# Optimization experiments

Hardware: AMD Instinct MI355X
Metric: run time of the kernel (lower is better)

## Reference

```python
import jax, jax.numpy as jnp
import numpy as np

B, SQ, SK, D, H = 2, 2048, 2048, 1024, 16
DK = D // H


def setup_inputs() -> dict:
    key = jax.random.key(0)
    ks = jax.random.split(key, 9)
    query = jax.random.normal(ks[0], (B, SQ, D), dtype=jnp.float32)
    k_in = jax.random.normal(ks[1], (B, SK, D), dtype=jnp.float32)
    v_in = jax.random.normal(ks[2], (B, SK, D), dtype=jnp.float32)
    # padding mask: 1 for valid tokens, 0 for padding; lengths in [SK//2, SK]
    lengths = jax.random.randint(ks[3], (B,), SK // 2, SK + 1)
    mask = (jnp.arange(SK)[None, :] < lengths[:, None]).astype(jnp.int32)
    scale = 1.0 / np.sqrt(D)
    Wq = jax.random.normal(ks[4], (D, D), dtype=jnp.float32) * scale
    Wk = jax.random.normal(ks[5], (D, D), dtype=jnp.float32) * scale
    Wv = jax.random.normal(ks[6], (D, D), dtype=jnp.float32) * scale
    Wo = jax.random.normal(ks[7], (D, D), dtype=jnp.float32) * scale
    return {"query": query, "key": k_in, "value": v_in, "mask": mask,
            "Wq": Wq, "Wk": Wk, "Wv": Wv, "Wo": Wo}


def reference(query, key, value, mask, Wq, Wk, Wv, Wo):
    # linear projections (torch Linear: x @ W.T)
    q = (query @ Wq.T).reshape(B, SQ, H, DK).transpose(0, 2, 1, 3)  # [B,H,SQ,DK]
    k = (key @ Wk.T).reshape(B, SK, H, DK).transpose(0, 2, 1, 3)    # [B,H,SK,DK]
    v = (value @ Wv.T).reshape(B, SK, H, DK).transpose(0, 2, 1, 3)  # [B,H,SK,DK]
    scores = jnp.einsum('bhqd,bhkd->bhqk', q, k) / jnp.sqrt(jnp.float32(DK))
    # padding mask: (B, SK) -> (B, 1, 1, SK)
    scores = jnp.where(mask[:, None, None, :] == 0, -jnp.inf, scores)
    # future (causal) mask
    future = jnp.triu(jnp.ones((SQ, SK), dtype=bool), k=1)
    scores = jnp.where(future[None, None], -jnp.inf, scores)
    attn = jax.nn.softmax(scores, axis=-1)
    attn = jnp.nan_to_num(attn, nan=0.0)
    ctx = jnp.einsum('bhqk,bhkd->bhqd', attn, v)
    ctx = ctx.transpose(0, 2, 1, 3).reshape(B, SQ, D)
    return ctx @ Wo.T
```

## Files before the change

kernel.cpp:

```cpp
#include <hip/hip_runtime.h>
#include <hip/hip_bf16.h>
#include <stdint.h>

#define BB 2
#define SS 2048
#define DD 1024
#define HH 16
#define DKK 64
#define MM (BB*SS)
#define LOG2E 1.4426950408889634f
#define QSCALE (0.125f * LOG2E)

typedef __attribute__((ext_vector_type(8))) short short8;
typedef __attribute__((ext_vector_type(8))) _Float16 half8;
typedef __attribute__((ext_vector_type(4))) float f32x4;

__device__ __forceinline__ short bfr(float f) {
    return (short)((__float_as_uint(f) + 0x8000u) >> 16);
}
__device__ __forceinline__ short f2h(float f) {
    _Float16 h = (_Float16)f;
    return __builtin_bit_cast(short, h);
}
__device__ __forceinline__ short8 cvt8(float4 a, float4 b) {
    short8 s;
    s[0] = bfr(a.x); s[1] = bfr(a.y); s[2] = bfr(a.z); s[3] = bfr(a.w);
    s[4] = bfr(b.x); s[5] = bfr(b.y); s[6] = bfr(b.z); s[7] = bfr(b.w);
    return s;
}

__device__ __forceinline__ void dma16(const void* g, void* l) {
    __builtin_amdgcn_global_load_lds(
        (const __attribute__((address_space(1))) uint32_t*)g,
        (__attribute__((address_space(3))) uint32_t*)(uintptr_t)l, 16, 0, 0);
}


__global__ __launch_bounds__(256) void cvt_all(const float* __restrict__ q,
                                               const float* __restrict__ k,
                                               const float* __restrict__ v,
                                               const float* __restrict__ wq,
                                               const float* __restrict__ wk,
                                               const float* __restrict__ wv,
                                               const float* __restrict__ wo,
                                               const int* __restrict__ mask,
                                               short* __restrict__ dst,
                                               float* __restrict__ Fb) {
    const size_t nth = (size_t)gridDim.x * blockDim.x;
    const size_t tid = (size_t)blockIdx.x * blockDim.x + threadIdx.x;
    if (tid < BB * SS) Fb[tid] = mask[tid] ? 0.f : -30000.f;
    for (size_t i8 = tid; i8 < (1u << 21); i8 += nth) {
        const size_t e = i8 * 8;
        const float* s;
        size_t rel;
        if (e < 4194304)        { s = q; rel = e; }
        else if (e < 8388608)   { s = k; rel = e - 4194304; }
        else if (e < 12582912)  { s = v; rel = e - 8388608; }
        else {
            const size_t we = e - 12582912;
            s = (we < 1048576) ? wq : (we < 2097152) ? wk : (we < 3145728) ? wv : wo;
            rel = we & 1048575;
        }
        const float4* p = (const float4*)(s + rel);
        *(short8*)(dst + e) = cvt8(p[0], p[1]);
    }
}

__global__ __launch_bounds__(256) void qkv_lds(const short* __restrict__ Abf,
                                               const short* __restrict__ Wbf,
                                               short* __restrict__ Qb,
                                               short* __restrict__ Kb,
                                               short* __restrict__ Vtb) {
    __shared__ __align__(16) short SH[12288];
    short* As = SH;
    short* Ws = SH + 4096;
    const int z = blockIdx.z;
    const short* A = Abf + (size_t)z * 4194304;
    const short* W = Wbf + (size_t)z * 1048576;
    const int t = threadIdx.x, wave = t >> 6, lane = t & 63;
    const int la = lane & 15, quad = lane >> 4;
    const int wm = wave & 1, wn = wave >> 1;
    const int m0 = blockIdx.x * 64, n0 = blockIdx.y * 128;

    f32x4 acc[2][4];
    #pragma unroll
    for (int i = 0; i < 2; ++i)
        #pragma unroll
        for (int j = 0; j < 4; ++j) acc[i][j] = {0.f, 0.f, 0.f, 0.f};

    for (int k0 = 0; k0 < DD; k0 += 64) {
        #pragma unroll
        for (int j = 0; j < 2; ++j) {
            const int idx = j * 256 + t;
            const int row = idx >> 3, gc = (idx & 7) ^ (row & 7);
            dma16(A + (size_t)(m0 + row) * DD + k0 + gc * 8, As + idx * 8);
        }
        #pragma unroll
        for (int j = 0; j < 4; ++j) {
            const int idx = j * 256 + t;
            const int row = idx >> 3, gc = (idx & 7) ^ (row & 7);
            dma16(W + (size_t)(n0 + row) * DD + k0 + gc * 8, Ws + idx * 8);
        }
        __syncthreads();
        #pragma unroll
        for (int kh = 0; kh < 2; ++kh) {
            short8 af[2], bf[4];
            #pragma unroll
            for (int mt = 0; mt < 2; ++mt) {
                const int row = wm * 32 + mt * 16 + la;
                af[mt] = *(const short8*)&As[row * 64 + (((kh << 2) | quad) ^ (row & 7)) * 8];
            }
            #pragma unroll
            for (int nt = 0; nt < 4; ++nt) {
                const int row = wn * 64 + nt * 16 + la;
                bf[nt] = *(const short8*)&Ws[row * 64 + (((kh << 2) | quad) ^ (row & 7)) * 8];
            }
            #pragma unroll
            for (int mt = 0; mt < 2; ++mt)
                #pragma unroll
                for (int nt = 0; nt < 4; ++nt)
                    acc[mt][nt] = __builtin_amdgcn_mfma_f32_16x16x32_bf16(af[mt], bf[nt], acc[mt][nt], 0, 0, 0);
        }
        __syncthreads();
    }

    #pragma unroll
    for (int mt = 0; mt < 2; ++mt)
        #pragma unroll
        for (int nt = 0; nt < 4; ++nt)
            #pragma unroll
            for (int r = 0; r < 4; ++r) {
                const float v = acc[mt][nt][r];
                const int mr = wm * 32 + mt * 16 + quad * 4 + r;
                const int nc = wn * 64 + nt * 16 + la;
                if (z == 2) SH[nc * 68 + mr] = f2h(v);
                else        SH[mr * 132 + nc] = bfr(z == 0 ? v * QSCALE : v);
            }
    __syncthreads();

    const int b = m0 >> 11;
    #pragma unroll
    for (int p = 0; p < 4; ++p) {
        const int idx = p * 256 + t;
        if (z == 2) {
            const int rr = idx >> 3, c8 = (idx & 7) * 8;
            short8 val = *(const short8*)&SH[rr * 68 + c8];
            const int n = n0 + rr, h2 = n >> 6, dk = n & 63;
            const int s = (m0 & (SS - 1)) + c8;
            *(short8*)(Vtb + ((size_t)(b * HH + h2) * DKK + dk) * SS + s) = val;
        } else {
            const int rr = idx >> 4, c8 = (idx & 15) * 8;
            short8 val = *(const short8*)&SH[rr * 132 + c8];
            const int s = (m0 + rr) & (SS - 1);
            const int n = n0 + c8, h2 = n >> 6, dk = n & 63;
            short* Y = (z == 0) ? Qb : Kb;
            *(short8*)(Y + ((size_t)(b * HH + h2) * SS + s) * DKK + dk) = val;
        }
    }
}

__global__ __launch_bounds__(256) void attn6(const short* __restrict__ Q,
                                             const short* __restrict__ K,
                                             const short* __restrict__ Vt,
                                             const float* __restrict__ Fb,
                                             short* __restrict__ ctx) {
    const int b = blockIdx.z, h = blockIdx.y, x = blockIdx.x;
    const int qtH = 31 - x, qtL = x;
    const int t = threadIdx.x, wave = t >> 6, lane = t & 63;
    const int la = lane & 15, quad = lane >> 4;

    __shared__ __align__(16) short Ks[64 * 72];
    __shared__ __align__(16) short Vs[64 * 72];
    __shared__ __align__(16) short PsH[64 * 72];
    __shared__ __align__(16) short PsL[64 * 72];

    const size_t kbase = ((size_t)(b * HH + h) * SS) * DKK;
    const size_t vbase = ((size_t)(b * HH + h) * DKK) * SS;

    const short8 aqH0 = *(const short8*)(Q + kbase + (size_t)(qtH * 64 + wave * 16 + la) * DKK + quad * 8);
    const short8 aqH1 = *(const short8*)(Q + kbase + (size_t)(qtH * 64 + wave * 16 + la) * DKK + 32 + quad * 8);
    const short8 aqL0 = *(const short8*)(Q + kbase + (size_t)(qtL * 64 + wave * 16 + la) * DKK + quad * 8);
    const short8 aqL1 = *(const short8*)(Q + kbase + (size_t)(qtL * 64 + wave * 16 + la) * DKK + 32 + quad * 8);

    const int srow = t >> 2, scol = (t & 3) * 16;
    short8 kr[2], vr[2];
    auto loadG = [&](int kt) {
        const short* kp = K + kbase + (size_t)(kt * 64 + srow) * DKK + scol;
        kr[0] = ((const short8*)kp)[0]; kr[1] = ((const short8*)kp)[1];
        const short* vp = Vt + vbase + (size_t)srow * SS + kt * 64 + scol;
        vr[0] = ((const short8*)vp)[0]; vr[1] = ((const short8*)vp)[1];
    };
    auto storeL = [&]() {
        *(short8*)&Ks[srow * 72 + scol]     = kr[0];
        *(short8*)&Ks[srow * 72 + scol + 8] = kr[1];
        *(short8*)&Vs[srow * 72 + scol]     = vr[0];
        *(short8*)&Vs[srow * 72 + scol + 8] = vr[1];
    };

    float rsH[4] = {0.f, 0.f, 0.f, 0.f}, rsL[4] = {0.f, 0.f, 0.f, 0.f};
    f32x4 oH[4], oL[4];
    #pragma unroll
    for (int dc = 0; dc < 4; ++dc) {
        oH[dc] = {0.f, 0.f, 0.f, 0.f};
        oL[dc] = {0.f, 0.f, 0.f, 0.f};
    }

    loadG(0); storeL(); __syncthreads();

    for (int kt = 0; kt <= qtH; ++kt) {
        if (kt < qtH) loadG(kt + 1);
        const bool doL = (kt <= qtL);

        f32x4 sH[4], sL[4];
        #pragma unroll
        for (int ct = 0; ct < 4; ++ct) {
            short8 kb0 = *(const short8*)&Ks[(ct * 16 + la) * 72 + quad * 8];
            short8 kb1 = *(const short8*)&Ks[(ct * 16 + la) * 72 + 32 + quad * 8];
            sH[ct] = {0.f, 0.f, 0.f, 0.f};
            sH[ct] = __builtin_amdgcn_mfma_f32_16x16x32_bf16(aqH0, kb0, sH[ct], 0, 0, 0);
            sH[ct] = __builtin_amdgcn_mfma_f32_16x16x32_bf16(aqH1, kb1, sH[ct], 0, 0, 0);
            if (doL) {
                sL[ct] = {0.f, 0.f, 0.f, 0.f};
                sL[ct] = __builtin_amdgcn_mfma_f32_16x16x32_bf16(aqL0, kb0, sL[ct], 0, 0, 0);
                sL[ct] = __builtin_amdgcn_mfma_f32_16x16x32_bf16(aqL1, kb1, sL[ct], 0, 0, 0);
            }
        }

        {
            const bool diag = (kt == qtH);
            const bool padded = (kt >= 16);
            #pragma unroll
            for (int ct = 0; ct < 4; ++ct) {
                const int col = kt * 64 + ct * 16 + la;
                const float bias = padded ? Fb[b * SS + col] : 0.f;
                const int row0 = qtH * 64 + wave * 16 + quad * 4;
                #pragma unroll
                for (int r = 0; r < 4; ++r) {
                    float xv = sH[ct][r] + bias;
                    if (diag && col > row0 + r) xv = -30000.f;
                    const float p = exp2f(xv);
                    rsH[r] += p;
                    PsH[(wave * 16 + quad * 4 + r) * 72 + ct * 16 + la] = f2h(p);
                }
            }
        }
        if (doL) {
            const bool diag = (kt == qtL);
            #pragma unroll
            for (int ct = 0; ct < 4; ++ct) {
                const int col = kt * 64 + ct * 16 + la;
                const int row0 = qtL * 64 + wave * 16 + quad * 4;
                #pragma unroll
                for (int r = 0; r < 4; ++r) {
                    float xv = sL[ct][r];
                    if (diag && col > row0 + r) xv = -30000.f;
                    const float p = exp2f(xv);
                    rsL[r] += p;
                    PsL[(wave * 16 + quad * 4 + r) * 72 + ct * 16 + la] = f2h(p);
                }
            }
        }

        #pragma unroll
        for (int c2 = 0; c2 < 2; ++c2) {
            half8 paH = *(const half8*)&PsH[(wave * 16 + la) * 72 + c2 * 32 + quad * 8];
            half8 paL;
            if (doL) paL = *(const half8*)&PsL[(wave * 16 + la) * 72 + c2 * 32 + quad * 8];
            #pragma unroll
            for (int dc = 0; dc < 4; ++dc) {
                half8 vb = *(const half8*)&Vs[(dc * 16 + la) * 72 + c2 * 32 + quad * 8];
                oH[dc] = __builtin_amdgcn_mfma_f32_16x16x32_f16(paH, vb, oH[dc], 0, 0, 0);
                if (doL)
                    oL[dc] = __builtin_amdgcn_mfma_f32_16x16x32_f16(paL, vb, oL[dc], 0, 0, 0);
            }
        }

        if (kt < qtH) {
            __syncthreads();
            storeL();
            __syncthreads();
        }
    }

    #pragma unroll
    for (int r = 0; r < 4; ++r) {
        float v = rsH[r];
        v += __shfl_xor(v, 1, 64);
        v += __shfl_xor(v, 2, 64);
        v += __shfl_xor(v, 4, 64);
        v += __shfl_xor(v, 8, 64);
        const float inv = 1.0f / v;
        const int q = qtH * 64 + wave * 16 + quad * 4 + r;
        #pragma unroll
        for (int dc = 0; dc < 4; ++dc)
            ctx[((size_t)(b * SS + q) * DD) + h * DKK + dc * 16 + la] = bfr(oH[dc][r] * inv);
    }
    #pragma unroll
    for (int r = 0; r < 4; ++r) {
        float v = rsL[r];
        v += __shfl_xor(v, 1, 64);
        v += __shfl_xor(v, 2, 64);
        v += __shfl_xor(v, 4, 64);
        v += __shfl_xor(v, 8, 64);
        const float inv = 1.0f / v;
        const int q = qtL * 64 + wave * 16 + quad * 4 + r;
        #pragma unroll
        for (int dc = 0; dc < 4; ++dc)
            ctx[((size_t)(b * SS + q) * DD) + h * DKK + dc * 16 + la] = bfr(oL[dc][r] * inv);
    }
}

__global__ __launch_bounds__(256) void o_lds(const short* __restrict__ Ctx,
                                             const short* __restrict__ Wob,
                                             float* __restrict__ out) {
    __shared__ __align__(16) short As[64 * 64];
    __shared__ __align__(16) short Ws[64 * 64];
    const int t = threadIdx.x, wave = t >> 6, lane = t & 63;
    const int la = lane & 15, quad = lane >> 4;
    const int wm = wave & 1, wn = wave >> 1;
    const int m0 = blockIdx.x * 64, n0 = blockIdx.y * 64;

    f32x4 acc[2][2];
    #pragma unroll
    for (int i = 0; i < 2; ++i)
        #pragma unroll
        for (int j = 0; j < 2; ++j) acc[i][j] = {0.f, 0.f, 0.f, 0.f};

    for (int k0 = 0; k0 < DD; k0 += 64) {
        #pragma unroll
        for (int j = 0; j < 2; ++j) {
            const int idx = j * 256 + t;
            const int row = idx >> 3, gc = (idx & 7) ^ (row & 7);
            dma16(Ctx + (size_t)(m0 + row) * DD + k0 + gc * 8, (short*)As + idx * 8);
            dma16(Wob + (size_t)(n0 + row) * DD + k0 + gc * 8, (short*)Ws + idx * 8);
        }
        __syncthreads();
        #pragma unroll
        for (int kh = 0; kh < 2; ++kh) {
            short8 af[2], bf[2];
            #pragma unroll
            for (int mt = 0; mt < 2; ++mt) {
                const int row = wm * 32 + mt * 16 + la;
                af[mt] = *(const short8*)&As[row * 64 + (((kh << 2) | quad) ^ (row & 7)) * 8];
            }
            #pragma unroll
            for (int nt = 0; nt < 2; ++nt) {
                const int row = wn * 32 + nt * 16 + la;
                bf[nt] = *(const short8*)&Ws[row * 64 + (((kh << 2) | quad) ^ (row & 7)) * 8];
            }
            #pragma unroll
            for (int mt = 0; mt < 2; ++mt)
                #pragma unroll
                for (int nt = 0; nt < 2; ++nt)
                    acc[mt][nt] = __builtin_amdgcn_mfma_f32_16x16x32_bf16(af[mt], bf[nt], acc[mt][nt], 0, 0, 0);
        }
        __syncthreads();
    }

    #pragma unroll
    for (int mt = 0; mt < 2; ++mt)
        #pragma unroll
        for (int nt = 0; nt < 2; ++nt)
            #pragma unroll
            for (int r = 0; r < 4; ++r) {
                const int m = m0 + wm * 32 + mt * 16 + quad * 4 + r;
                const int n = n0 + wn * 32 + nt * 16 + la;
                out[(size_t)m * DD + n] = acc[mt][nt][r];
            }
}

__global__ __launch_bounds__(256) void qkv_gemm(const float* __restrict__ Aq,
                                                const float* __restrict__ Ak,
                                                const float* __restrict__ Av,
                                                const float* __restrict__ Wq,
                                                const float* __restrict__ Wk,
                                                const float* __restrict__ Wv,
                                                short* __restrict__ Qb,
                                                short* __restrict__ Kb,
                                                short* __restrict__ Vtb) {
    __shared__ __align__(16) short As[2][128][40];
    __shared__ __align__(16) short Ws[2][128][40];
    const int z = blockIdx.z;
    const float* A = (z == 0) ? Aq : (z == 1) ? Ak : Av;
    const float* W = (z == 0) ? Wq : (z == 1) ? Wk : Wv;
    short* Y = (z == 0) ? Qb : (z == 1) ? Kb : Vtb;
    const int t = threadIdx.x, wave = t >> 6, lane = t & 63;
    const int la = lane & 15, quad = lane >> 4;
    const int wm = wave & 1, wn = wave >> 1;
    const int m0 = blockIdx.x * 128, n0 = blockIdx.y * 128;
    const int srow = t >> 1, scol = (t & 1) * 16;
    f32x4 acc[4][4];
    #pragma unroll
    for (int i = 0; i < 4; ++i)
        #pragma unroll
        for (int j = 0; j < 4; ++j) acc[i][j] = {0.f, 0.f, 0.f, 0.f};
    float4 ar[4], wr[4];
    auto loadG = [&](int i) {
        const int k0 = i * 32;
        const float4* pa = (const float4*)(A + (size_t)(m0 + srow) * DD + k0 + scol);
        ar[0] = pa[0]; ar[1] = pa[1]; ar[2] = pa[2]; ar[3] = pa[3];
        const float4* pw = (const float4*)(W + (size_t)(n0 + srow) * DD + k0 + scol);
        wr[0] = pw[0]; wr[1] = pw[1]; wr[2] = pw[2]; wr[3] = pw[3];
    };
    auto storeL = [&](int buf) {
        *(short8*)&As[buf][srow][scol]     = cvt8(ar[0], ar[1]);
        *(short8*)&As[buf][srow][scol + 8] = cvt8(ar[2], ar[3]);
        *(short8*)&Ws[buf][srow][scol]     = cvt8(wr[0], wr[1]);
        *(short8*)&Ws[buf][srow][scol + 8] = cvt8(wr[2], wr[3]);
    };
    loadG(0); storeL(0); __syncthreads();
    const int NIT = DD / 32;
    for (int i = 0; i < NIT; ++i) {
        if (i + 1 < NIT) loadG(i + 1);
        const int buf = i & 1;
        short8 af[4], bfv[4];
        #pragma unroll
        for (int mt = 0; mt < 4; ++mt)
            af[mt] = *(const short8*)&As[buf][wm * 64 + mt * 16 + la][quad * 8];
        #pragma unroll
        for (int nt = 0; nt < 4; ++nt)
            bfv[nt] = *(const short8*)&Ws[buf][wn * 64 + nt * 16 + la][quad * 8];
        #pragma unroll
        for (int mt = 0; mt < 4; ++mt)
            #pragma unroll
            for (int nt = 0; nt < 4; ++nt)
                acc[mt][nt] = __builtin_amdgcn_mfma_f32_16x16x32_bf16(af[mt], bfv[nt], acc[mt][nt], 0, 0, 0);
        if (i + 1 < NIT) { storeL((i + 1) & 1); __syncthreads(); }
    }
    #pragma unroll
    for (int mt = 0; mt < 4; ++mt)
        #pragma unroll
        for (int nt = 0; nt < 4; ++nt)
            #pragma unroll
            for (int r = 0; r < 4; ++r) {
                const int m = m0 + wm * 64 + mt * 16 + quad * 4 + r;
                const int n = n0 + wn * 64 + nt * 16 + la;
                const int b = m >> 11, s = m & (SS - 1);
                const int h = n >> 6, dk = n & 63;
                float v = acc[mt][nt][r];
                if (z == 0)      Y[(((size_t)(b * HH + h) * SS + s) * DKK) + dk] = bfr(v * QSCALE);
                else if (z == 1) Y[(((size_t)(b * HH + h) * SS + s) * DKK) + dk] = bfr(v);
                else             Y[(((size_t)(b * HH + h) * DKK + dk) * SS) + s] = bfr(v);
            }
}

__global__ __launch_bounds__(256) void attn_fused(const short* __restrict__ Q,
                                                  const short* __restrict__ K,
                                                  const short* __restrict__ Vt,
                                                  const int* __restrict__ mask,
                                                  short* __restrict__ ctx) {
    const int b = blockIdx.z, h = blockIdx.y, x = blockIdx.x;
    const int t = threadIdx.x, wave = t >> 6, lane = t & 63;
    const int la = lane & 15, quad = lane >> 4;
    __shared__ __align__(16) short Ks[2][64][72];
    __shared__ __align__(16) short Vs[2][64][72];
    __shared__ __align__(16) short Ps[64][72];
    const size_t kbase = ((size_t)(b * HH + h) * SS) * DKK;
    const size_t vbase = ((size_t)(b * HH + h) * DKK) * SS;
    const int srow = t >> 2, scol = (t & 3) * 16;
    short8 kr[2], vr[2];
    auto loadG = [&](int kt) {
        const short* kp = K + kbase + (size_t)(kt * 64 + srow) * DKK + scol;
        kr[0] = ((const short8*)kp)[0]; kr[1] = ((const short8*)kp)[1];
        const short* vp = Vt + vbase + (size_t)srow * SS + kt * 64 + scol;
        vr[0] = ((const short8*)vp)[0]; vr[1] = ((const short8*)vp)[1];
    };
    auto storeL = [&](int buf) {
        *(short8*)&Ks[buf][srow][scol]     = kr[0];
        *(short8*)&Ks[buf][srow][scol + 8] = kr[1];
        *(short8*)&Vs[buf][srow][scol]     = vr[0];
        *(short8*)&Vs[buf][srow][scol + 8] = vr[1];
    };
    #pragma unroll 1
    for (int phase = 0; phase < 2; ++phase) {
        const int qt = phase ? x : (31 - x);
        const size_t qbase = kbase + (size_t)(qt * 64) * DKK;
        const short8 aq0 = *(const short8*)(Q + qbase + (size_t)(wave * 16 + la) * DKK + quad * 8);
        const short8 aq1 = *(const short8*)(Q + qbase + (size_t)(wave * 16 + la) * DKK + 32 + quad * 8);
        float rs[4] = {0.f, 0.f, 0.f, 0.f};
        f32x4 o[4];
        #pragma unroll
        for (int dc = 0; dc < 4; ++dc) o[dc] = {0.f, 0.f, 0.f, 0.f};
        const int nkt = qt + 1;
        loadG(0); storeL(0); __syncthreads();
        for (int kt = 0; kt < nkt; ++kt) {
            if (kt + 1 < nkt) loadG(kt + 1);
            const int buf = kt & 1;
            const bool diag = (kt == qt);
            const bool padded = (kt >= 16);
            f32x4 s[4];
            #pragma unroll
            for (int ct = 0; ct < 4; ++ct) {
                s[ct] = {0.f, 0.f, 0.f, 0.f};
                short8 kb0 = *(const short8*)&Ks[buf][ct * 16 + la][quad * 8];
                short8 kb1 = *(const short8*)&Ks[buf][ct * 16 + la][32 + quad * 8];
                s[ct] = __builtin_amdgcn_mfma_f32_16x16x32_bf16(aq0, kb0, s[ct], 0, 0, 0);
                s[ct] = __builtin_amdgcn_mfma_f32_16x16x32_bf16(aq1, kb1, s[ct], 0, 0, 0);
            }
            const int rowq = qt * 64 + wave * 16 + quad * 4;
            #pragma unroll
            for (int ct = 0; ct < 4; ++ct) {
                const int col = kt * 64 + ct * 16 + la;
                const int mv = padded ? mask[b * SS + col] : 1;
                #pragma unroll
                for (int r = 0; r < 4; ++r) {
                    const bool dead = (diag && col > rowq + r) || (padded && mv == 0);
                    const float p = dead ? 0.f : exp2f(s[ct][r]);
                    rs[r] += p;
                    Ps[wave * 16 + quad * 4 + r][ct * 16 + la] = bfr(p);
                }
            }
            #pragma unroll
            for (int c2 = 0; c2 < 2; ++c2) {
                short8 pa = *(const short8*)&Ps[wave * 16 + la][c2 * 32 + quad * 8];
                #pragma unroll
                for (int dc = 0; dc < 4; ++dc) {
                    short8 vb = *(const short8*)&Vs[buf][dc * 16 + la][c2 * 32 + quad * 8];
                    o[dc] = __builtin_amdgcn_mfma_f32_16x16x32_bf16(pa, vb, o[dc], 0, 0, 0);
                }
            }
            if (kt + 1 < nkt) { storeL((kt + 1) & 1); __syncthreads(); }
        }
        #pragma unroll
        for (int r = 0; r < 4; ++r) {
            float v = rs[r];
            v += __shfl_xor(v, 1, 64);
            v += __shfl_xor(v, 2, 64);
            v += __shfl_xor(v, 4, 64);
            v += __shfl_xor(v, 8, 64);
            const float inv = 1.0f / v;
            const int q = qt * 64 + wave * 16 + quad * 4 + r;
            #pragma unroll
            for (int dc = 0; dc < 4; ++dc)
                ctx[((size_t)(b * SS + q) * DD) + h * DKK + dc * 16 + la] = bfr(o[dc][r] * inv);
        }
        __syncthreads();
    }
}

__global__ __launch_bounds__(256) void o_gemm(const short* __restrict__ Ctx,
                                              const float* __restrict__ Wo,
                                              float* __restrict__ out) {
    __shared__ __align__(16) short As[2][128][40];
    __shared__ __align__(16) short Ws[2][64][40];
    const int t = threadIdx.x, wave = t >> 6, lane = t & 63;
    const int la = lane & 15, quad = lane >> 4;
    const int wm = wave & 1, wn = wave >> 1;
    const int m0 = blockIdx.x * 128, n0 = blockIdx.y * 64;
    const int srowA = t >> 1, scolA = (t & 1) * 16;
    const int srowW = t >> 2, scolW = (t & 3) * 8;
    f32x4 acc[4][2];
    #pragma unroll
    for (int i = 0; i < 4; ++i)
        #pragma unroll
        for (int j = 0; j < 2; ++j) acc[i][j] = {0.f, 0.f, 0.f, 0.f};
    short8 ab[2];
    float4 wr[2];
    auto loadG = [&](int i) {
        const int k0 = i * 32;
        const short8* pa = (const short8*)(Ctx + (size_t)(m0 + srowA) * DD + k0 + scolA);
        ab[0] = pa[0]; ab[1] = pa[1];
        const float4* pw = (const float4*)(Wo + (size_t)(n0 + srowW) * DD + k0 + scolW);
        wr[0] = pw[0]; wr[1] = pw[1];
    };
    auto storeL = [&](int buf) {
        *(short8*)&As[buf][srowA][scolA]     = ab[0];
        *(short8*)&As[buf][srowA][scolA + 8] = ab[1];
        *(short8*)&Ws[buf][srowW][scolW]     = cvt8(wr[0], wr[1]);
    };
    loadG(0); storeL(0); __syncthreads();
    const int NIT = DD / 32;
    for (int i = 0; i < NIT; ++i) {
        if (i + 1 < NIT) loadG(i + 1);
        const int buf = i & 1;
        short8 af[4], bfv[2];
        #pragma unroll
        for (int mt = 0; mt < 4; ++mt)
            af[mt] = *(const short8*)&As[buf][wm * 64 + mt * 16 + la][quad * 8];
        #pragma unroll
        for (int nt = 0; nt < 2; ++nt)
            bfv[nt] = *(const short8*)&Ws[buf][wn * 32 + nt * 16 + la][quad * 8];
        #pragma unroll
        for (int mt = 0; mt < 4; ++mt)
            #pragma unroll
            for (int nt = 0; nt < 2; ++nt)
                acc[mt][nt] = __builtin_amdgcn_mfma_f32_16x16x32_bf16(af[mt], bfv[nt], acc[mt][nt], 0, 0, 0);
        if (i + 1 < NIT) { storeL((i + 1) & 1); __syncthreads(); }
    }
    #pragma unroll
    for (int mt = 0; mt < 4; ++mt)
        #pragma unroll
        for (int nt = 0; nt < 2; ++nt)
            #pragma unroll
            for (int r = 0; r < 4; ++r) {
                const int m = m0 + wm * 64 + mt * 16 + quad * 4 + r;
                const int n = n0 + wn * 32 + nt * 16 + la;
                out[(size_t)m * DD + n] = acc[mt][nt][r];
            }
}

extern "C" void kernel_launch(void* const* d_in, const int* in_sizes, int n_in,
                              void* d_out, int out_size, void* d_ws, size_t ws_size,
                              hipStream_t stream) {
    (void)in_sizes; (void)n_in; (void)out_size;
    const float* query = (const float*)d_in[0];
    const float* key   = (const float*)d_in[1];
    const float* value = (const float*)d_in[2];
    const int*   mask  = (const int*)  d_in[3];
    const float* Wq    = (const float*)d_in[4];
    const float* Wk    = (const float*)d_in[5];
    const float* Wv    = (const float*)d_in[6];
    const float* Wo    = (const float*)d_in[7];
    dim3 tb(256);

    if (ws_size >= (size_t)61000000) {
        short* Abf = (short*)d_ws;
        short* Wbf = Abf + 12582912;
        short* Qb  = Abf + 16777216;
        short* Kb  = Abf + 20971520;
        short* Vtb = Abf + 25165824;
        float* Fb  = (float*)(Abf + 29360128);
        short* Ctx = Abf;

        hipLaunchKernelGGL(cvt_all, dim3(1024), tb, 0, stream,
                           query, key, value, Wq, Wk, Wv, Wo, mask, Abf, Fb);
        hipLaunchKernelGGL(qkv_lds, dim3(64, 8, 3), tb, 0, stream, Abf, Wbf, Qb, Kb, Vtb);
        hipLaunchKernelGGL(attn6, dim3(16, 16, 2), tb, 0, stream,
                           (const short*)Qb, (const short*)Kb, (const short*)Vtb, Fb, Ctx);
        hipLaunchKernelGGL(o_lds, dim3(64, 16), tb, 0, stream,
                           (const short*)Ctx, (const short*)(Wbf + 3145728), (float*)d_out);
    } else {
        short* Qb  = (short*)d_ws;
        short* Kb  = Qb + (size_t)BB * HH * SS * DKK;
        short* Vtb = Kb + (size_t)BB * HH * SS * DKK;
        short* Ctx = Vtb + (size_t)BB * HH * SS * DKK;
        hipLaunchKernelGGL(qkv_gemm, dim3(MM / 128, DD / 128, 3), tb, 0, stream,
                           query, key, value, Wq, Wk, Wv, Qb, Kb, Vtb);
        hipLaunchKernelGGL(attn_fused, dim3(SS / 128, HH, BB), tb, 0, stream,
                           (const short*)Qb, (const short*)Kb, (const short*)Vtb, mask, Ctx);
        hipLaunchKernelGGL(o_gemm, dim3(MM / 128, DD / 64), tb, 0, stream,
                           (const short*)Ctx, Wo, (float*)d_out);
    }
}
```

Measured before the change: 233.3 us.

## Split attention KV loop across two blocks and combine partial sums

Each attention block now processes only every other KV tile (even or odd split), doubling the grid from 512 to 1024 blocks. Unnormalized partial outputs (bf16) and row sums are written to scratch, and a new combine kernel adds the two halves, normalizes, and writes ctx in the original layout. This targets low occupancy and parallelism on a 256-CU GPU at the cost of an extra kernel launch, extra global traffic, and bf16 rounding of unnormalized partials. It relies on the existing softmax having no running max, so partials combine by simple addition.

```diff
diff --git a/kernel.cpp b/kernel.cpp
--- a/kernel.cpp
+++ b/kernel.cpp
@@ -17,6 +17,9 @@
 
 __device__ __forceinline__ short bfr(float f) {
     return (short)((__float_as_uint(f) + 0x8000u) >> 16);
+}
+__device__ __forceinline__ float b2f(short s) {
+    return __uint_as_float(((uint32_t)(uint16_t)s) << 16);
 }
 __device__ __forceinline__ short f2h(float f) {
     _Float16 h = (_Float16)f;
@@ -159,23 +162,27 @@
     }
 }
 
-__global__ __launch_bounds__(256) void attn6(const short* __restrict__ Q,
+__global__ __launch_bounds__(256) void attn8(const short* __restrict__ Q,
                                              const short* __restrict__ K,
                                              const short* __restrict__ Vt,
                                              const float* __restrict__ Fb,
-                                             short* __restrict__ ctx) {
-    const int b = blockIdx.z, h = blockIdx.y, x = blockIdx.x;
+                                             short* __restrict__ Op,
+                                             float* __restrict__ Lp) {
+    const int b = blockIdx.z, h = blockIdx.y;
+    const int sp = blockIdx.x & 1;
+    const int x  = blockIdx.x >> 1;
     const int qtH = 31 - x, qtL = x;
     const int t = threadIdx.x, wave = t >> 6, lane = t & 63;
     const int la = lane & 15, quad = lane >> 4;
+    const int bh = b * HH + h;
 
     __shared__ __align__(16) short Ks[64 * 72];
     __shared__ __align__(16) short Vs[64 * 72];
     __shared__ __align__(16) short PsH[64 * 72];
     __shared__ __align__(16) short PsL[64 * 72];
 
-    const size_t kbase = ((size_t)(b * HH + h) * SS) * DKK;
-    const size_t vbase = ((size_t)(b * HH + h) * DKK) * SS;
+    const size_t kbase = ((size_t)bh * SS) * DKK;
+    const size_t vbase = ((size_t)bh * DKK) * SS;
 
     const short8 aqH0 = *(const short8*)(Q + kbase + (size_t)(qtH * 64 + wave * 16 + la) * DKK + quad * 8);
     const short8 aqH1 = *(const short8*)(Q + kbase + (size_t)(qtH * 64 + wave * 16 + la) * DKK + 32 + quad * 8);
@@ -205,10 +212,12 @@
         oL[dc] = {0.f, 0.f, 0.f, 0.f};
     }
 
-    loadG(0); storeL(); __syncthreads();
-
-    for (int kt = 0; kt <= qtH; ++kt) {
-        if (kt < qtH) loadG(kt + 1);
+    if (sp <= qtH) {
+        loadG(sp); storeL(); __syncthreads();
+    }
+
+    for (int kt = sp; kt <= qtH; kt += 2) {
+        if (kt + 2 <= qtH) loadG(kt + 2);
         const bool doL = (kt <= qtL);
 
         f32x4 sH[4], sL[4];
@@ -229,11 +238,11 @@
         {
             const bool diag = (kt == qtH);
             const bool padded = (kt >= 16);
+            const int row0 = qtH * 64 + wave * 16 + quad * 4;
             #pragma unroll
             for (int ct = 0; ct < 4; ++ct) {
                 const int col = kt * 64 + ct * 16 + la;
                 const float bias = padded ? Fb[b * SS + col] : 0.f;
-                const int row0 = qtH * 64 + wave * 16 + quad * 4;
                 #pragma unroll
                 for (int r = 0; r < 4; ++r) {
                     float xv = sH[ct][r] + bias;
@@ -246,10 +255,10 @@
         }
         if (doL) {
             const bool diag = (kt == qtL);
+            const int row0 = qtL * 64 + wave * 16 + quad * 4;
             #pragma unroll
             for (int ct = 0; ct < 4; ++ct) {
                 const int col = kt * 64 + ct * 16 + la;
-                const int row0 = qtL * 64 + wave * 16 + quad * 4;
                 #pragma unroll
                 for (int r = 0; r < 4; ++r) {
                     float xv = sL[ct][r];
@@ -275,13 +284,14 @@
             }
         }
 
-        if (kt < qtH) {
+        if (kt + 2 <= qtH) {
             __syncthreads();
             storeL();
             __syncthreads();
         }
     }
 
+    const size_t obase = ((size_t)(sp * BB * HH + bh) * SS);
     #pragma unroll
     for (int r = 0; r < 4; ++r) {
         float v = rsH[r];
@@ -289,11 +299,11 @@
         v += __shfl_xor(v, 2, 64);
         v += __shfl_xor(v, 4, 64);
         v += __shfl_xor(v, 8, 64);
-        const float inv = 1.0f / v;
         const int q = qtH * 64 + wave * 16 + quad * 4 + r;
+        if (la == 0) Lp[obase + q] = v;
         #pragma unroll
         for (int dc = 0; dc < 4; ++dc)
-            ctx[((size_t)(b * SS + q) * DD) + h * DKK + dc * 16 + la] = bfr(oH[dc][r] * inv);
+            Op[(obase + q) * DKK + dc * 16 + la] = bfr(oH[dc][r]);
     }
     #pragma unroll
     for (int r = 0; r < 4; ++r) {
@@ -302,12 +312,29 @@
         v += __shfl_xor(v, 2, 64);
         v += __shfl_xor(v, 4, 64);
         v += __shfl_xor(v, 8, 64);
-        const float inv = 1.0f / v;
         const int q = qtL * 64 + wave * 16 + quad * 4 + r;
+        if (la == 0) Lp[obase + q] = v;
         #pragma unroll
         for (int dc = 0; dc < 4; ++dc)
-            ctx[((size_t)(b * SS + q) * DD) + h * DKK + dc * 16 + la] = bfr(oL[dc][r] * inv);
-    }
+            Op[(obase + q) * DKK + dc * 16 + la] = bfr(oL[dc][r]);
+    }
+}
+
+__global__ __launch_bounds__(256) void attn_combine(const short* __restrict__ Op,
+                                                    const float* __restrict__ Lp,
+                                                    short* __restrict__ ctx) {
+    const size_t i8 = (size_t)blockIdx.x * blockDim.x + threadIdx.x;
+    const int row = (int)(i8 >> 3);
+    const int c8 = ((int)i8 & 7) * 8;
+    const float inv = 1.0f / (Lp[row] + Lp[BB * HH * SS + row]);
+    short8 a = *(const short8*)(Op + (size_t)row * DKK + c8);
+    short8 bq = *(const short8*)(Op + (size_t)(BB * HH * SS + row) * DKK + c8);
+    short8 o;
+    #pragma unroll
+    for (int i = 0; i < 8; ++i) o[i] = bfr((b2f(a[i]) + b2f(bq[i])) * inv);
+    const int bh = row >> 11, s = row & (SS - 1);
+    const int b = bh >> 4, h = bh & 15;
+    *(short8*)(ctx + ((size_t)(b * SS + s) * DD) + h * DKK + c8) = o;
 }
 
 __global__ __launch_bounds__(256) void o_lds(const short* __restrict__ Ctx,
@@ -620,13 +647,17 @@
         short* Kb  = Abf + 20971520;
         short* Vtb = Abf + 25165824;
         float* Fb  = (float*)(Abf + 29360128);
-        short* Ctx = Abf;
+        float* Lp  = (float*)(Abf + 29368320);
+        short* Op  = Abf;
+        short* Ctx = Abf + 8388608;
 
         hipLaunchKernelGGL(cvt_all, dim3(1024), tb, 0, stream,
                            query, key, value, Wq, Wk, Wv, Wo, mask, Abf, Fb);
         hipLaunchKernelGGL(qkv_lds, dim3(64, 8, 3), tb, 0, stream, Abf, Wbf, Qb, Kb, Vtb);
-        hipLaunchKernelGGL(attn6, dim3(16, 16, 2), tb, 0, stream,
-                           (const short*)Qb, (const short*)Kb, (const short*)Vtb, Fb, Ctx);
+        hipLaunchKernelGGL(attn8, dim3(32, 16, 2), tb, 0, stream,
+                           (const short*)Qb, (const short*)Kb, (const short*)Vtb, Fb, Op, Lp);
+        hipLaunchKernelGGL(attn_combine, dim3(2048), tb, 0, stream,
+                           (const short*)Op, (const float*)Lp, Ctx);
         hipLaunchKernelGGL(o_lds, dim3(64, 16), tb, 0, stream,
                            (const short*)Ctx, (const short*)(Wbf + 3145728), (float*)d_out);
     } else {
```

New measurement: 255.4 us. +9.5%, slower.
